# Performance work log

Measured on AMD Instinct MI355X. Metric: run time of the kernel, lower is better.

The kernel has to match this reference:

```python
import jax, jax.numpy as jnp
import numpy as np

N_NODES = 100_000
N_EDGES = 2_500_000
HID = 32
SE3_NORM = 1.0 / np.sqrt(32.0)  # e3nn path normalization for 32x0e -> 32x0e


def setup_inputs() -> dict:
    key = jax.random.key(0)
    ks = jax.random.split(key, 14)
    inp = {
        "pos": jax.random.normal(ks[0], (N_NODES, 3), dtype=jnp.float32),
        "edge_index": jax.random.randint(ks[1], (2, N_EDGES), 0, N_NODES, dtype=jnp.int64),
        "Wl1": jax.random.normal(ks[2], (2, HID), dtype=jnp.float32) * 0.5,
        "bl1": jax.random.normal(ks[3], (HID,), dtype=jnp.float32) * 0.1,
        "Wr1": jax.random.normal(ks[4], (2, HID), dtype=jnp.float32) * 0.5,
        "Wl2": jax.random.normal(ks[5], (HID, HID), dtype=jnp.float32) * 0.15,
        "bl2": jax.random.normal(ks[6], (HID,), dtype=jnp.float32) * 0.1,
        "Wr2": jax.random.normal(ks[7], (HID, HID), dtype=jnp.float32) * 0.15,
        "Wse1": jax.random.normal(ks[8], (HID, HID), dtype=jnp.float32) * 0.15,
        "Wse2": jax.random.normal(ks[9], (HID, HID), dtype=jnp.float32) * 0.15,
        "W3": jax.random.normal(ks[10], (HID, HID), dtype=jnp.float32) * 0.15,
        "b3": jax.random.normal(ks[11], (HID,), dtype=jnp.float32) * 0.1,
        "W4": jax.random.normal(ks[12], (HID, 1), dtype=jnp.float32) * 0.15,
        "b4": jax.random.normal(ks[13], (1,), dtype=jnp.float32) * 0.1,
        "alpha": jnp.float32(0.5),
    }
    return inp


def _sage_conv(x, src, dst, Wl, bl, Wr, n_nodes):
    # gather messages from source nodes, scatter-sum onto destination nodes
    agg = jax.ops.segment_sum(x[src], dst, num_segments=n_nodes)  # [N, d_in]
    return agg @ Wl + bl + x @ Wr  # lin_l(agg) + lin_r(x); lin_r has no bias


def reference(pos, edge_index, Wl1, bl1, Wr1, Wl2, bl2, Wr2, Wse1, Wse2, W3, b3, W4, b4, alpha):
    n = pos.shape[0]
    x = pos[:, :2]                       # [N, 2]
    src, dst = edge_index[0], edge_index[1]

    h1 = _sage_conv(x, src, dst, Wl1, bl1, Wr1, n)   # [N, 32]
    h1 = jax.nn.leaky_relu(h1, negative_slope=0.01)  # dropout = identity (eval)
    h1 = (h1 @ Wse1) * SE3_NORM                      # SE3Linear 32x0e->32x0e

    h2 = _sage_conv(h1, src, dst, Wl2, bl2, Wr2, n)
    h2 = jax.nn.leaky_relu(h2, negative_slope=0.01)
    h2 = (h2 @ Wse2) * SE3_NORM

    x_skip = alpha * h1 + h2
    x_out = jax.nn.relu(x_skip @ W3 + b3)            # mlp3 (dropout identity)
    pred = x_out @ W4 + b4                           # mlp4
    return pred.squeeze(-1)                          # [N]
```

## Files before the change

### kernel.cpp

```cpp
#include <hip/hip_runtime.h>
#include <hip/hip_fp16.h>

#define HID 32
#define LEAKY 0.01f
#define SE3NORM 0.17677669529663687f
#define SCAN_TILE 1024
#define NBK 128
#define GA 256
#define NPB2 64


__global__ void k_bhist(const int* __restrict__ ei, int* __restrict__ bh,
                        int E, int B1, int chunk) {
    extern __shared__ int lh[];
    int g = blockIdx.x;
    for (int i = threadIdx.x; i < B1; i += 256) lh[i] = 0;
    __syncthreads();
    int beg = g * chunk, end = min(E, beg + chunk);
    for (int e = beg + (int)threadIdx.x; e < end; e += 256)
        atomicAdd(&lh[__builtin_nontemporal_load(&ei[E + e]) >> 7], 1);
    __syncthreads();
    for (int b = threadIdx.x; b < B1; b += 256) bh[b * GA + g] = lh[b];
}

__global__ void k_scan1(int* __restrict__ data, int* __restrict__ bsum, int M) {
    __shared__ int lds[256];
    int t = threadIdx.x;
    int base = blockIdx.x * SCAN_TILE + t * 4;
    int v0 = (base + 0 < M) ? data[base + 0] : 0;
    int v1 = (base + 1 < M) ? data[base + 1] : 0;
    int v2 = (base + 2 < M) ? data[base + 2] : 0;
    int v3 = (base + 3 < M) ? data[base + 3] : 0;
    int s = v0 + v1 + v2 + v3;
    lds[t] = s;
    __syncthreads();
    for (int off = 1; off < 256; off <<= 1) {
        int x = (t >= off) ? lds[t - off] : 0;
        __syncthreads();
        lds[t] += x;
        __syncthreads();
    }
    int ex = lds[t] - s;
    if (base + 0 < M) data[base + 0] = ex;
    if (base + 1 < M) data[base + 1] = ex + v0;
    if (base + 2 < M) data[base + 2] = ex + v0 + v1;
    if (base + 3 < M) data[base + 3] = ex + v0 + v1 + v2;
    if (t == 255) bsum[blockIdx.x] = lds[255];
}

__global__ void k_scan2(int* __restrict__ bsum, int B) {
    __shared__ int lds[256];
    int t = threadIdx.x;
    int v = (t < B) ? bsum[t] : 0;
    lds[t] = v;
    __syncthreads();
    for (int off = 1; off < 256; off <<= 1) {
        int x = (t >= off) ? lds[t - off] : 0;
        __syncthreads();
        lds[t] += x;
        __syncthreads();
    }
    if (t < B) bsum[t] = lds[t] - v;
}

__global__ void k_scan3(int* __restrict__ data, const int* __restrict__ bsum,
                        int* __restrict__ cursor, int M, int N) {
    int i = blockIdx.x * blockDim.x + threadIdx.x;
    if (i >= M) return;
    int off = data[i] + bsum[i / SCAN_TILE];
    data[i] = off;
    if (cursor && i < N) cursor[i] = off;
}

__global__ void k_bscatter(const int* __restrict__ ei, const int* __restrict__ bh,
                           int* __restrict__ bucketed, int E, int B1, int chunk) {
    extern __shared__ int cur[];
    int g = blockIdx.x;
    for (int b = threadIdx.x; b < B1; b += 256) cur[b] = bh[b * GA + g];
    __syncthreads();
    int beg = g * chunk, end = min(E, beg + chunk);
    for (int e = beg + (int)threadIdx.x; e < end; e += 256) {
        int d = __builtin_nontemporal_load(&ei[E + e]);
        int s = __builtin_nontemporal_load(&ei[e]);
        int b = d >> 7;
        int p = atomicAdd(&cur[b], 1);
        bucketed[p] = s | ((d & (NBK - 1)) << 24);
    }
}

__global__ __launch_bounds__(256, 1) void k_bsort_node1(
        const int* __restrict__ bh, const int* __restrict__ bucketed,
        const float* __restrict__ pos,
        const float* __restrict__ Wl1, const float* __restrict__ bl1,
        const float* __restrict__ Wr1, const float* __restrict__ Wse1,
        int* __restrict__ sorted_src, int* __restrict__ offsets,
        __half* __restrict__ h1, int E, int N, int B1) {
    __shared__ int hist[NBK], sc[NBK], base[NBK];
    __shared__ float aggx[NBK], aggy[NBK];
    __shared__ float sWl1[2 * HID], sWr1[2 * HID], sbl1[HID], sWse1[HID * HID];
    __shared__ float sH[32][HID + 4];
    const int b = blockIdx.x;
    const int t = threadIdx.x;
    for (int i = t; i < 2 * HID; i += 256) { sWl1[i] = Wl1[i]; sWr1[i] = Wr1[i]; }
    for (int i = t; i < HID; i += 256) sbl1[i] = bl1[i];
    for (int i = t; i < HID * HID; i += 256) sWse1[i] = Wse1[i];
    const int bs = bh[b * GA];
    const int be = (b == B1 - 1) ? E : bh[(b + 1) * GA];
    if (t < NBK) { hist[t] = 0; aggx[t] = 0.f; aggy[t] = 0.f; }
    __syncthreads();
    for (int e = bs + t; e < be; e += 256) {
        int pv = bucketed[e];
        int dl = pv >> 24;
        int s = pv & 0x00FFFFFF;
        atomicAdd(&hist[dl], 1);
        atomicAdd(&aggx[dl], pos[s * 3]);
        atomicAdd(&aggy[dl], pos[s * 3 + 1]);
    }
    __syncthreads();
    int v = (t < NBK) ? hist[t] : 0;
    if (t < NBK) sc[t] = v;
    __syncthreads();
    for (int off = 1; off < NBK; off <<= 1) {
        int x = (t < NBK && t >= off) ? sc[t - off] : 0;
        __syncthreads();
        if (t < NBK) sc[t] += x;
        __syncthreads();
    }
    if (t < NBK) base[t] = sc[t] - v;
    __syncthreads();
    if (t < NBK) hist[t] = base[t];
    __syncthreads();
    for (int e = bs + t; e < be; e += 256) {
        int pv = bucketed[e];
        int p = atomicAdd(&hist[pv >> 24], 1);
        sorted_src[bs + p] = pv & 0x00FFFFFF;
    }
    int nodeg = b * NBK + t;
    if (t < NBK && nodeg < N) offsets[nodeg] = bs + base[t];
    if (b == B1 - 1 && t == 0) offsets[N] = E;
    __syncthreads();
    const int nodeL = t >> 3;
    const int lane = t & 7;
    for (int c = 0; c < NBK / 32; c++) {
        const int dl = c * 32 + nodeL;
        const int node = b * NBK + dl;
        const bool live = node < N;
        if (live) {
            float a0 = aggx[dl], a1 = aggy[dl];
            float x0 = pos[3 * node], x1 = pos[3 * node + 1];
#pragma unroll
            for (int jj = 0; jj < 4; jj++) {
                int k = lane * 4 + jj;
                float vv = a0 * sWl1[k] + a1 * sWl1[HID + k] + sbl1[k]
                         + x0 * sWr1[k] + x1 * sWr1[HID + k];
                sH[nodeL][k] = vv > 0.f ? vv : LEAKY * vv;
            }
        }
        __syncthreads();
        if (live) {
            float4 acc = make_float4(0.f, 0.f, 0.f, 0.f);
#pragma unroll 8
            for (int k = 0; k < HID; k++) {
                float hk = sH[nodeL][k];
                float4 w = *(const float4*)&sWse1[k * HID + lane * 4];
                acc.x += hk * w.x; acc.y += hk * w.y;
                acc.z += hk * w.z; acc.w += hk * w.w;
            }
            union Pack4 { __half h[4]; float2 v; } p;
            p.h[0] = __float2half(acc.x * SE3NORM);
            p.h[1] = __float2half(acc.y * SE3NORM);
            p.h[2] = __float2half(acc.z * SE3NORM);
            p.h[3] = __float2half(acc.w * SE3NORM);
            *(float2*)&h1[(size_t)node * HID + lane * 4] = p.v;
        }
        __syncthreads();
    }
}

__global__ void k_hist_rank(const int* __restrict__ ei, int* __restrict__ hist,
                            int* __restrict__ rank, int E) {
    int base = (blockIdx.x * blockDim.x + threadIdx.x) * 4;
#pragma unroll
    for (int u = 0; u < 4; u++) {
        int e = base + u;
        if (e < E) rank[e] = atomicAdd(&hist[ei[E + e]], 1);
    }
}
__global__ void k_hist(const int* __restrict__ ei, int* __restrict__ hist, int E) {
    int base = (blockIdx.x * blockDim.x + threadIdx.x) * 4;
#pragma unroll
    for (int u = 0; u < 4; u++) {
        int e = base + u;
        if (e < E) atomicAdd(&hist[ei[E + e]], 1);
    }
}
__global__ void k_scatter_rank(const int* __restrict__ ei, const int* __restrict__ offsets,
                               const int* __restrict__ rank, int* __restrict__ sorted_src, int E) {
    int base = (blockIdx.x * blockDim.x + threadIdx.x) * 4;
#pragma unroll
    for (int u = 0; u < 4; u++) {
        int e = base + u;
        if (e < E) sorted_src[offsets[ei[E + e]] + rank[e]] = ei[e];
    }
}
__global__ void k_scatter_atomic(const int* __restrict__ ei, int* __restrict__ cursor,
                                 int* __restrict__ sorted_src, int E) {
    int base = (blockIdx.x * blockDim.x + threadIdx.x) * 4;
#pragma unroll
    for (int u = 0; u < 4; u++) {
        int e = base + u;
        if (e < E) {
            int p = atomicAdd(&cursor[ei[E + e]], 1);
            sorted_src[p] = ei[e];
        }
    }
}

__global__ __launch_bounds__(256, 1) void k_node1(
                        const int* __restrict__ offsets, const int* __restrict__ sorted_src,
                        const float* __restrict__ pos,
                        const float* __restrict__ Wl1, const float* __restrict__ bl1,
                        const float* __restrict__ Wr1, const float* __restrict__ Wse1,
                        __half* __restrict__ h1, int N) {
    __shared__ float sWl1[2 * HID], sWr1[2 * HID], sbl1[HID], sWse1[HID * HID];
    __shared__ float sH[32][HID + 4];
    for (int i = threadIdx.x; i < 2 * HID; i += blockDim.x) { sWl1[i] = Wl1[i]; sWr1[i] = Wr1[i]; }
    for (int i = threadIdx.x; i < HID; i += blockDim.x) sbl1[i] = bl1[i];
    for (int i = threadIdx.x; i < HID * HID; i += blockDim.x) sWse1[i] = Wse1[i];
    __syncthreads();

    const int lt = threadIdx.x;
    const int nodeL = lt >> 3;
    const int t = lt & 7;
    const int node = blockIdx.x * 32 + nodeL;
    const bool live = node < N;

    float a0 = 0.f, a1 = 0.f;
    if (live) {
        int beg = offsets[node], end = offsets[node + 1];
        for (int e = beg + t; e < end; e += 8) {
            int s = sorted_src[e];
            a0 += pos[s * 3];
            a1 += pos[s * 3 + 1];
        }
    }
    a0 += __shfl_xor(a0, 1); a1 += __shfl_xor(a1, 1);
    a0 += __shfl_xor(a0, 2); a1 += __shfl_xor(a1, 2);
    a0 += __shfl_xor(a0, 4); a1 += __shfl_xor(a1, 4);

    if (live) {
        float x0 = pos[3 * node], x1 = pos[3 * node + 1];
#pragma unroll
        for (int jj = 0; jj < 4; jj++) {
            int k = t * 4 + jj;
            float v = a0 * sWl1[k] + a1 * sWl1[HID + k] + sbl1[k] + x0 * sWr1[k] + x1 * sWr1[HID + k];
            sH[nodeL][k] = v > 0.f ? v : LEAKY * v;
        }
    }
    __syncthreads();

    if (live) {
        float4 acc = make_float4(0.f, 0.f, 0.f, 0.f);
#pragma unroll 8
        for (int k = 0; k < HID; k++) {
            float hk = sH[nodeL][k];
            float4 w = *(const float4*)&sWse1[k * HID + t * 4];
            acc.x += hk * w.x; acc.y += hk * w.y;
            acc.z += hk * w.z; acc.w += hk * w.w;
        }
        union Pack4 { __half h[4]; float2 v; } p;
        p.h[0] = __float2half(acc.x * SE3NORM);
        p.h[1] = __float2half(acc.y * SE3NORM);
        p.h[2] = __float2half(acc.z * SE3NORM);
        p.h[3] = __float2half(acc.w * SE3NORM);
        *(float2*)&h1[(size_t)node * HID + t * 4] = p.v;
    }
}

__device__ __forceinline__ void acc_h1frag(float2 r, float4& acc) {
    __half2 p01 = __builtin_bit_cast(__half2, r.x);
    __half2 p23 = __builtin_bit_cast(__half2, r.y);
    acc.x += __low2float(p01); acc.y += __high2float(p01);
    acc.z += __low2float(p23); acc.w += __high2float(p23);
}

__global__ __launch_bounds__(512, 1) void k_node2out(
                           const int* __restrict__ offsets, const int* __restrict__ sorted_src,
                           const __half* __restrict__ h1,
                           const float* __restrict__ Wl2, const float* __restrict__ bl2,
                           const float* __restrict__ Wr2, const float* __restrict__ Wse2,
                           const float* __restrict__ W3, const float* __restrict__ b3,
                           const float* __restrict__ W4, const float* __restrict__ b4,
                           const float* __restrict__ alpha_p,
                           float* __restrict__ out, int N) {
    __shared__ float sWl2[HID * HID], sWr2[HID * HID], sWse2[HID * HID], sW3[HID * HID];
    __shared__ float sbl2[HID], sb3[HID], sW4[HID];
    __shared__ float sb4, salpha;
    __shared__ float sA[NPB2][HID + 4], sB[NPB2][HID + 4];
    for (int i = threadIdx.x; i < HID * HID; i += blockDim.x) {
        sWl2[i] = Wl2[i]; sWr2[i] = Wr2[i]; sWse2[i] = Wse2[i]; sW3[i] = W3[i];
    }
    for (int i = threadIdx.x; i < HID; i += blockDim.x) { sbl2[i] = bl2[i]; sb3[i] = b3[i]; sW4[i] = W4[i]; }
    if (threadIdx.x == 0) { sb4 = b4[0]; salpha = alpha_p[0]; }
    __syncthreads();

    const int lt = threadIdx.x;
    const int nodeL = lt >> 3;
    const int t = lt & 7;
    const int node = blockIdx.x * NPB2 + nodeL;
    const bool live = node < N;

    if (live) {
        float2 ro = *(const float2*)&h1[(size_t)node * HID + t * 4];

        int beg = offsets[node], end = offsets[node + 1];
        float4 acc = make_float4(0.f, 0.f, 0.f, 0.f);
        int e = beg;
        for (; e + 8 <= end; e += 8) {
            int s0 = __builtin_nontemporal_load(&sorted_src[e + 0]);
            int s1 = __builtin_nontemporal_load(&sorted_src[e + 1]);
            int s2 = __builtin_nontemporal_load(&sorted_src[e + 2]);
            int s3 = __builtin_nontemporal_load(&sorted_src[e + 3]);
            int s4 = __builtin_nontemporal_load(&sorted_src[e + 4]);
            int s5 = __builtin_nontemporal_load(&sorted_src[e + 5]);
            int s6 = __builtin_nontemporal_load(&sorted_src[e + 6]);
            int s7 = __builtin_nontemporal_load(&sorted_src[e + 7]);
            float2 r0 = *(const float2*)&h1[(size_t)s0 * HID + t * 4];
            float2 r1 = *(const float2*)&h1[(size_t)s1 * HID + t * 4];
            float2 r2 = *(const float2*)&h1[(size_t)s2 * HID + t * 4];
            float2 r3 = *(const float2*)&h1[(size_t)s3 * HID + t * 4];
            float2 r4 = *(const float2*)&h1[(size_t)s4 * HID + t * 4];
            float2 r5 = *(const float2*)&h1[(size_t)s5 * HID + t * 4];
            float2 r6 = *(const float2*)&h1[(size_t)s6 * HID + t * 4];
            float2 r7 = *(const float2*)&h1[(size_t)s7 * HID + t * 4];
            acc_h1frag(r0, acc); acc_h1frag(r1, acc);
            acc_h1frag(r2, acc); acc_h1frag(r3, acc);
            acc_h1frag(r4, acc); acc_h1frag(r5, acc);
            acc_h1frag(r6, acc); acc_h1frag(r7, acc);
        }
        for (; e < end; e++) {
            int s = __builtin_nontemporal_load(&sorted_src[e]);
            float2 r = *(const float2*)&h1[(size_t)s * HID + t * 4];
            acc_h1frag(r, acc);
        }
        __half2 o01 = __builtin_bit_cast(__half2, ro.x);
        __half2 o23 = __builtin_bit_cast(__half2, ro.y);
        float4 own = make_float4(__low2float(o01), __high2float(o01),
                                 __low2float(o23), __high2float(o23));
        *(float4*)&sA[nodeL][t * 4] = acc;
        *(float4*)&sB[nodeL][t * 4] = own;
    }
    __syncthreads();

    float h2r[4];
    if (live) {
        h2r[0] = sbl2[t * 4 + 0]; h2r[1] = sbl2[t * 4 + 1];
        h2r[2] = sbl2[t * 4 + 2]; h2r[3] = sbl2[t * 4 + 3];
#pragma unroll 8
        for (int k = 0; k < HID; k++) {
            float a = sA[nodeL][k];
            float b = sB[nodeL][k];
            float4 wl = *(const float4*)&sWl2[k * HID + t * 4];
            float4 wr = *(const float4*)&sWr2[k * HID + t * 4];
            h2r[0] += a * wl.x + b * wr.x;
            h2r[1] += a * wl.y + b * wr.y;
            h2r[2] += a * wl.z + b * wr.z;
            h2r[3] += a * wl.w + b * wr.w;
        }
#pragma unroll
        for (int jj = 0; jj < 4; jj++) h2r[jj] = h2r[jj] > 0.f ? h2r[jj] : LEAKY * h2r[jj];
    }
    __syncthreads();
    if (live) {
        float4 st = make_float4(h2r[0], h2r[1], h2r[2], h2r[3]);
        *(float4*)&sA[nodeL][t * 4] = st;
    }
    __syncthreads();

    if (live) {
        float4 acc = make_float4(0.f, 0.f, 0.f, 0.f);
#pragma unroll 8
        for (int k = 0; k < HID; k++) {
            float a = sA[nodeL][k];
            float4 w = *(const float4*)&sWse2[k * HID + t * 4];
            acc.x += a * w.x; acc.y += a * w.y;
            acc.z += a * w.z; acc.w += a * w.w;
        }
        float4 own = *(const float4*)&sB[nodeL][t * 4];
        own.x = salpha * own.x + acc.x * SE3NORM;
        own.y = salpha * own.y + acc.y * SE3NORM;
        own.z = salpha * own.z + acc.z * SE3NORM;
        own.w = salpha * own.w + acc.w * SE3NORM;
        *(float4*)&sB[nodeL][t * 4] = own;
    }
    __syncthreads();

    float acc4[4];
    acc4[0] = sb3[t * 4 + 0]; acc4[1] = sb3[t * 4 + 1];
    acc4[2] = sb3[t * 4 + 2]; acc4[3] = sb3[t * 4 + 3];
    if (live) {
#pragma unroll 8
        for (int k = 0; k < HID; k++) {
            float s = sB[nodeL][k];
            float4 w = *(const float4*)&sW3[k * HID + t * 4];
            acc4[0] += s * w.x; acc4[1] += s * w.y;
            acc4[2] += s * w.z; acc4[3] += s * w.w;
        }
    }
    float part = 0.f;
#pragma unroll
    for (int jj = 0; jj < 4; jj++)
        part += (acc4[jj] > 0.f ? acc4[jj] : 0.f) * sW4[t * 4 + jj];
    part += __shfl_xor(part, 1);
    part += __shfl_xor(part, 2);
    part += __shfl_xor(part, 4);
    if (live && t == 0) out[node] = part + sb4;
}

extern "C" void kernel_launch(void* const* d_in, const int* in_sizes, int n_in,
                              void* d_out, int out_size, void* d_ws, size_t ws_size,
                              hipStream_t stream) {
    const float* pos  = (const float*)d_in[0];
    const int*   ei   = (const int*)d_in[1];
    const float* Wl1  = (const float*)d_in[2];
    const float* bl1  = (const float*)d_in[3];
    const float* Wr1  = (const float*)d_in[4];
    const float* Wl2  = (const float*)d_in[5];
    const float* bl2  = (const float*)d_in[6];
    const float* Wr2  = (const float*)d_in[7];
    const float* Wse1 = (const float*)d_in[8];
    const float* Wse2 = (const float*)d_in[9];
    const float* W3   = (const float*)d_in[10];
    const float* b3   = (const float*)d_in[11];
    const float* W4   = (const float*)d_in[12];
    const float* b4   = (const float*)d_in[13];
    const float* alp  = (const float*)d_in[14];
    float* out = (float*)d_out;

    const int N = in_sizes[0] / 3;
    const int E = in_sizes[1] / 2;
    const int blk = 256;
    const size_t h1bytes = (size_t)N * HID * sizeof(__half);

    const int B1 = (N + NBK - 1) / NBK;
    const int M2 = B1 * GA;
    const int S2 = (M2 + SCAN_TILE - 1) / SCAN_TILE;
    {
        int* bh         = (int*)d_ws;
        int* bsum       = bh + M2;
        int* bucketed   = bsum + 256;
        int* sorted_src = bucketed + E;
        int* offsets    = sorted_src + E;
        uintptr_t hp = ((uintptr_t)(offsets + N + 1) + 15) & ~(uintptr_t)15;
        size_t need = (hp - (uintptr_t)d_ws) + h1bytes;
        if (need <= ws_size && S2 <= 256) {
            __half* h1 = (__half*)hp;
            const int chunk = (E + GA - 1) / GA;
            const size_t ldsB = (size_t)B1 * sizeof(int);
            k_bhist<<<GA, 256, ldsB, stream>>>(ei, bh, E, B1, chunk);
            k_scan1<<<S2, 256, 0, stream>>>(bh, bsum, M2);
            k_scan2<<<1, 256, 0, stream>>>(bsum, S2);
            k_scan3<<<(M2 + blk - 1) / blk, blk, 0, stream>>>(bh, bsum, nullptr, M2, 0);
            k_bscatter<<<GA, 256, ldsB, stream>>>(ei, bh, bucketed, E, B1, chunk);
            k_bsort_node1<<<B1, 256, 0, stream>>>(bh, bucketed, pos,
                                                  Wl1, bl1, Wr1, Wse1,
                                                  sorted_src, offsets, h1, E, N, B1);
            k_node2out<<<(N + NPB2 - 1) / NPB2, 512, 0, stream>>>(offsets, sorted_src, h1,
                                                          Wl2, bl2, Wr2, Wse2,
                                                          W3, b3, W4, b4, alp, out, N);
            return;
        }
    }

    const int M = N + 1;
    const int B = (M + SCAN_TILE - 1) / SCAN_TILE;
    int* hist       = (int*)d_ws;
    int* offsets    = hist + M;
    int* bsum       = offsets + M;
    int* sorted_src = bsum + 256;
    int* aux        = sorted_src + E;
    uintptr_t hpA = ((uintptr_t)(aux + E) + 15) & ~(uintptr_t)15;
    uintptr_t hpB = ((uintptr_t)(aux + N) + 15) & ~(uintptr_t)15;
    size_t needA = (hpA - (uintptr_t)d_ws) + h1bytes;
    const bool useRank = (needA <= ws_size);
    __half* h1 = (__half*)(useRank ? hpA : hpB);

    hipMemsetAsync(hist, 0, (size_t)M * sizeof(int), stream);
    const int egrid4 = (E / 4 + blk) / blk;
    if (useRank) {
        k_hist_rank<<<egrid4, blk, 0, stream>>>(ei, hist, aux, E);
    } else {
        k_hist<<<egrid4, blk, 0, stream>>>(ei, hist, E);
    }
    k_scan1<<<B, 256, 0, stream>>>(hist, bsum, M);
    k_scan2<<<1, 256, 0, stream>>>(bsum, B);
    k_scan3<<<(M + blk - 1) / blk, blk, 0, stream>>>(hist, bsum, useRank ? nullptr : aux, M, N);
    int* offs = hist;
    if (useRank) {
        k_scatter_rank<<<egrid4, blk, 0, stream>>>(ei, offs, aux, sorted_src, E);
    } else {
        k_scatter_atomic<<<egrid4, blk, 0, stream>>>(ei, aux, sorted_src, E);
    }
    k_node1<<<(N + 31) / 32, 256, 0, stream>>>(offs, sorted_src, pos, Wl1, bl1, Wr1, Wse1, h1, N);
    k_node2out<<<(N + NPB2 - 1) / NPB2, 512, 0, stream>>>(offs, sorted_src, h1, Wl2, bl2, Wr2, Wse2,
                                                  W3, b3, W4, b4, alp, out, N);
}
```

Baseline: 281.8 us.

## Split layer-1 node compute out of bucket sort into separate k_node1 kernel

Removes the fused layer-1 aggregation and node transform from the bucket-sort kernel, leaving k_bsort to only build sorted_src and offsets. A separate k_node1 launch then computes h1 from the CSR arrays. This drops the float LDS atomics and the serial per-block node loop under launch_bounds(256,1), at the cost of an extra launch and re-reading sorted_src. Nontemporal loads of edge_index are also replaced by plain loads.

```diff
diff --git a/kernel.cpp b/kernel.cpp
--- a/kernel.cpp
+++ b/kernel.cpp
@@ -18,7 +18,7 @@
     __syncthreads();
     int beg = g * chunk, end = min(E, beg + chunk);
     for (int e = beg + (int)threadIdx.x; e < end; e += 256)
-        atomicAdd(&lh[__builtin_nontemporal_load(&ei[E + e]) >> 7], 1);
+        atomicAdd(&lh[ei[E + e] >> 7], 1);
     __syncthreads();
     for (int b = threadIdx.x; b < B1; b += 256) bh[b * GA + g] = lh[b];
 }
@@ -80,42 +80,26 @@
     __syncthreads();
     int beg = g * chunk, end = min(E, beg + chunk);
     for (int e = beg + (int)threadIdx.x; e < end; e += 256) {
-        int d = __builtin_nontemporal_load(&ei[E + e]);
-        int s = __builtin_nontemporal_load(&ei[e]);
+        int d = ei[E + e];
+        int s = ei[e];
         int b = d >> 7;
         int p = atomicAdd(&cur[b], 1);
         bucketed[p] = s | ((d & (NBK - 1)) << 24);
     }
 }
 
-__global__ __launch_bounds__(256, 1) void k_bsort_node1(
-        const int* __restrict__ bh, const int* __restrict__ bucketed,
-        const float* __restrict__ pos,
-        const float* __restrict__ Wl1, const float* __restrict__ bl1,
-        const float* __restrict__ Wr1, const float* __restrict__ Wse1,
-        int* __restrict__ sorted_src, int* __restrict__ offsets,
-        __half* __restrict__ h1, int E, int N, int B1) {
+__global__ void k_bsort(const int* __restrict__ bh, const int* __restrict__ bucketed,
+                        int* __restrict__ sorted_src, int* __restrict__ offsets,
+                        int E, int N, int B1) {
     __shared__ int hist[NBK], sc[NBK], base[NBK];
-    __shared__ float aggx[NBK], aggy[NBK];
-    __shared__ float sWl1[2 * HID], sWr1[2 * HID], sbl1[HID], sWse1[HID * HID];
-    __shared__ float sH[32][HID + 4];
-    const int b = blockIdx.x;
-    const int t = threadIdx.x;
-    for (int i = t; i < 2 * HID; i += 256) { sWl1[i] = Wl1[i]; sWr1[i] = Wr1[i]; }
-    for (int i = t; i < HID; i += 256) sbl1[i] = bl1[i];
-    for (int i = t; i < HID * HID; i += 256) sWse1[i] = Wse1[i];
-    const int bs = bh[b * GA];
-    const int be = (b == B1 - 1) ? E : bh[(b + 1) * GA];
-    if (t < NBK) { hist[t] = 0; aggx[t] = 0.f; aggy[t] = 0.f; }
-    __syncthreads();
-    for (int e = bs + t; e < be; e += 256) {
-        int pv = bucketed[e];
-        int dl = pv >> 24;
-        int s = pv & 0x00FFFFFF;
-        atomicAdd(&hist[dl], 1);
-        atomicAdd(&aggx[dl], pos[s * 3]);
-        atomicAdd(&aggy[dl], pos[s * 3 + 1]);
-    }
+    int b = blockIdx.x;
+    int t = threadIdx.x;
+    int bs = bh[b * GA];
+    int be = (b == B1 - 1) ? E : bh[(b + 1) * GA];
+    if (t < NBK) hist[t] = 0;
+    __syncthreads();
+    for (int e = bs + t; e < be; e += 256)
+        atomicAdd(&hist[bucketed[e] >> 24], 1);
     __syncthreads();
     int v = (t < NBK) ? hist[t] : 0;
     if (t < NBK) sc[t] = v;
@@ -135,46 +119,9 @@
         int p = atomicAdd(&hist[pv >> 24], 1);
         sorted_src[bs + p] = pv & 0x00FFFFFF;
     }
-    int nodeg = b * NBK + t;
-    if (t < NBK && nodeg < N) offsets[nodeg] = bs + base[t];
+    int node = b * NBK + t;
+    if (t < NBK && node < N) offsets[node] = bs + base[t];
     if (b == B1 - 1 && t == 0) offsets[N] = E;
-    __syncthreads();
-    const int nodeL = t >> 3;
-    const int lane = t & 7;
-    for (int c = 0; c < NBK / 32; c++) {
-        const int dl = c * 32 + nodeL;
-        const int node = b * NBK + dl;
-        const bool live = node < N;
-        if (live) {
-            float a0 = aggx[dl], a1 = aggy[dl];
-            float x0 = pos[3 * node], x1 = pos[3 * node + 1];
-#pragma unroll
-            for (int jj = 0; jj < 4; jj++) {
-                int k = lane * 4 + jj;
-                float vv = a0 * sWl1[k] + a1 * sWl1[HID + k] + sbl1[k]
-                         + x0 * sWr1[k] + x1 * sWr1[HID + k];
-                sH[nodeL][k] = vv > 0.f ? vv : LEAKY * vv;
-            }
-        }
-        __syncthreads();
-        if (live) {
-            float4 acc = make_float4(0.f, 0.f, 0.f, 0.f);
-#pragma unroll 8
-            for (int k = 0; k < HID; k++) {
-                float hk = sH[nodeL][k];
-                float4 w = *(const float4*)&sWse1[k * HID + lane * 4];
-                acc.x += hk * w.x; acc.y += hk * w.y;
-                acc.z += hk * w.z; acc.w += hk * w.w;
-            }
-            union Pack4 { __half h[4]; float2 v; } p;
-            p.h[0] = __float2half(acc.x * SE3NORM);
-            p.h[1] = __float2half(acc.y * SE3NORM);
-            p.h[2] = __float2half(acc.z * SE3NORM);
-            p.h[3] = __float2half(acc.w * SE3NORM);
-            *(float2*)&h1[(size_t)node * HID + lane * 4] = p.v;
-        }
-        __syncthreads();
-    }
 }
 
 __global__ void k_hist_rank(const int* __restrict__ ei, int* __restrict__ hist,
@@ -462,9 +409,9 @@
             k_scan2<<<1, 256, 0, stream>>>(bsum, S2);
             k_scan3<<<(M2 + blk - 1) / blk, blk, 0, stream>>>(bh, bsum, nullptr, M2, 0);
             k_bscatter<<<GA, 256, ldsB, stream>>>(ei, bh, bucketed, E, B1, chunk);
-            k_bsort_node1<<<B1, 256, 0, stream>>>(bh, bucketed, pos,
-                                                  Wl1, bl1, Wr1, Wse1,
-                                                  sorted_src, offsets, h1, E, N, B1);
+            k_bsort<<<B1, 256, 0, stream>>>(bh, bucketed, sorted_src, offsets, E, N, B1);
+            k_node1<<<(N + 31) / 32, 256, 0, stream>>>(offsets, sorted_src, pos,
+                                                       Wl1, bl1, Wr1, Wse1, h1, N);
             k_node2out<<<(N + NPB2 - 1) / NPB2, 512, 0, stream>>>(offsets, sorted_src, h1,
                                                           Wl2, bl2, Wr2, Wse2,
                                                           W3, b3, W4, b4, alp, out, N);
```

Measured after the change: 244.3 us. 1.15x faster.
